# Kernel tuning notes

Measured on AMD Instinct MI355X. Metric: run time of the kernel, lower is better.

The kernel has to match this reference:

```python
import jax, jax.numpy as jnp
import numpy as np

BIAS_VALUE = -1e30


def apply_rope(inputs, positions, max_wavelength=10000):
    # inputs: [B, T, H, Dh]; positions: [B, T]
    head_dim = inputs.shape[-1]
    fraction = 2 * jnp.arange(0, head_dim // 2) / head_dim
    timescale = max_wavelength ** fraction
    sinusoid_inp = positions[..., jnp.newaxis] / timescale[jnp.newaxis, :]  # [B, T, Dh/2]
    sinusoid_inp = sinusoid_inp[..., jnp.newaxis, :]                        # [B, T, 1, Dh/2]
    sin = jnp.sin(sinusoid_inp)
    cos = jnp.cos(sinusoid_inp)
    first_half, second_half = jnp.split(inputs, 2, axis=-1)
    first_part = first_half * cos - second_half * sin
    second_part = second_half * cos + first_half * sin
    return jnp.concatenate([first_part, second_part], axis=-1).astype(inputs.dtype)


def rms_norm(x, scale):
    var = jnp.mean(jnp.square(x), axis=-1, keepdims=True)
    return x * jax.lax.rsqrt(var + 1e-6) * (1 + scale)


def setup_inputs() -> dict:
    key = jax.random.key(0)
    ks = jax.random.split(key, 12)
    B, T, D, H, Dh = 4, 2048, 512, 8, 64
    q = jax.random.normal(ks[0], (B, T, D), jnp.float32)
    kv = jax.random.normal(ks[1], (B, T, D), jnp.float32)
    mask = jnp.broadcast_to(jnp.tril(jnp.ones((T, T), bool))[None, None], (B, 1, T, T))
    pos = jnp.broadcast_to(jnp.arange(T, dtype=jnp.int32), (B, T))
    s = 0.02
    return {
        "q": q, "kv": kv, "mask": mask, "q_positions": pos, "kv_positions": pos,
        "wq": jax.random.normal(ks[2], (D, H * Dh), jnp.float32) * s,
        "bq": jnp.zeros((H * Dh,), jnp.float32),
        "wk": jax.random.normal(ks[3], (D, H * Dh), jnp.float32) * s,
        "bk": jnp.zeros((H * Dh,), jnp.float32),
        "wv": jax.random.normal(ks[4], (D, H * Dh), jnp.float32) * s,
        "bv": jnp.zeros((H * Dh,), jnp.float32),
        "scale_q": jax.random.normal(ks[5], (Dh,), jnp.float32) * s,
        "scale_k": jax.random.normal(ks[6], (Dh,), jnp.float32) * s,
        "wo": jax.random.normal(ks[7], (H * Dh, D), jnp.float32) * s,
        "bo": jnp.zeros((D,), jnp.float32),
    }


def reference(q, kv, mask, q_positions, kv_positions,
              wq, bq, wk, bk, wv, bv, scale_q, scale_k, wo, bo):
    B, T, D = q.shape
    H = 8
    Dh = wq.shape[1] // H
    qk_size = Dh

    def proj(x, w, b):
        y = x @ w + b
        return y.reshape(*x.shape[:-1], H, -1)  # [B, T, H, Dh]

    query_heads = rms_norm(proj(q, wq, bq), scale_q)
    key_heads = rms_norm(proj(kv, wk, bk), scale_k)
    value_heads = proj(kv, wv, bv)

    query_heads = apply_rope(query_heads, q_positions)
    key_heads = apply_rope(key_heads, kv_positions)

    attn_logits = jnp.einsum('bthd,bThd->bhtT', query_heads, key_heads)
    attn_logits = attn_logits / np.sqrt(qk_size).astype(q.dtype)
    attn_logits = jnp.where(mask, attn_logits, BIAS_VALUE)
    attn_weights = jax.nn.softmax(attn_logits, axis=-1)
    attn_weights = jnp.where(mask, attn_weights, 0)
    attn = jnp.einsum('bhtT,bThd->bthd', attn_weights, value_heads)
    attn = attn.reshape(B, T, -1)
    return attn @ wo + bo
```

## Files before the change

### kernel.cpp

```cpp
#include <hip/hip_runtime.h>
#include <hip/hip_bf16.h>
#include <cstdint>

#define B_ 4
#define T_ 2048
#define D_ 512
#define H_ 8

typedef __bf16 bf16x8 __attribute__((ext_vector_type(8)));
typedef __bf16 bf16x4 __attribute__((ext_vector_type(4)));
typedef float f32x4 __attribute__((ext_vector_type(4)));

#define QSCALE 0.18033688011112042f
#define MSHIFT 16.0f

__device__ inline void gload_lds16(const void* g, void* l) {
    __builtin_amdgcn_global_load_lds(
        (const __attribute__((address_space(1))) void*)g,
        (__attribute__((address_space(3))) void*)l, 16, 0, 0);
}

__global__ void cast2_kernel(const float* __restrict__ qf, const float* __restrict__ kvf,
                             __bf16* __restrict__ qb, __bf16* __restrict__ kvb, int n4) {
    int stride = gridDim.x * blockDim.x;
    for (int i = blockIdx.x * blockDim.x + threadIdx.x; i < 2 * n4; i += stride) {
        const float* src = (i < n4) ? qf : kvf;
        __bf16* dst = (i < n4) ? qb : kvb;
        int j = (i < n4) ? i : i - n4;
        float4 v = reinterpret_cast<const float4*>(src)[j];
        bf16x4 o = { (__bf16)v.x, (__bf16)v.y, (__bf16)v.z, (__bf16)v.w };
        reinterpret_cast<bf16x4*>(dst)[j] = o;
    }
}

__global__ void transpose_w4_kernel(const float* __restrict__ wq, const float* __restrict__ wk,
                                    const float* __restrict__ wv, const float* __restrict__ wo,
                                    __bf16* __restrict__ wqkvT, __bf16* __restrict__ woT) {
    __shared__ float tile[32][33];
    int z = blockIdx.z;
    const float* in = (z == 0) ? wq : (z == 1) ? wk : (z == 2) ? wv : wo;
    __bf16* out = (z < 3) ? wqkvT + (size_t)z * D_ * D_ : woT;
    int tx = threadIdx.x & 31, ty = threadIdx.x >> 5;
    int r0 = blockIdx.y * 32, c0 = blockIdx.x * 32;
#pragma unroll
    for (int i = 0; i < 4; i++)
        tile[ty + i * 8][tx] = in[(size_t)(r0 + ty + i * 8) * D_ + c0 + tx];
    __syncthreads();
#pragma unroll
    for (int i = 0; i < 4; i++)
        out[(size_t)(c0 + ty + i * 8) * D_ + r0 + tx] = (__bf16)tile[tx][ty + i * 8];
}

__global__ void rope_table_kernel(float2* __restrict__ tab) {
    int i = blockIdx.x * 256 + threadIdx.x;
    int p = i >> 5, d2 = i & 31;
    float inv_ts = exp2f((float)d2 * (-13.28771237954945f / 32.0f));
    float ang = (float)p * inv_ts;
    float sv, cv;
    __sincosf(ang, &sv, &cv);
    tab[i] = make_float2(cv, sv);
}

template<int MODE>
__global__ __launch_bounds__(256, 2) void gemm_tile_kernel(
    const __bf16* __restrict__ Xq, const __bf16* __restrict__ Xkv,
    const __bf16* __restrict__ WT,
    const float* __restrict__ biasQ, const float* __restrict__ biasK,
    const float* __restrict__ biasV,
    float* __restrict__ outf, __bf16* __restrict__ qh, __bf16* __restrict__ kh,
    __bf16* __restrict__ vt,
    const float* __restrict__ scale_q, const float* __restrict__ scale_k,
    const int* __restrict__ qpos, const int* __restrict__ kpos,
    const float2* __restrict__ rtab, int M, int Ntot, int K) {
    __shared__ __bf16 Ab[2][128 * 32];
    __shared__ __bf16 Bb[2][128 * 32];

    const int tid = threadIdx.x;
    const int lane = tid & 63, widx = tid >> 6;
    const int lo = lane & 15, hi = lane >> 4;
    const int wm = widx >> 1, wn = widx & 1;

    const int nwg = gridDim.x;
    const int q8 = nwg >> 3;
    int bid = blockIdx.x;
    int swz = (bid & 7) * q8 + (bid >> 3);
    const int ntn = Ntot >> 7;
    const int m0 = (swz / ntn) << 7;
    const int nt = swz % ntn;
    const int n0g = nt << 7;
    const int seg = (MODE == 3) ? (nt >> 2) : 0;
    const __bf16* X = (MODE == 3 && seg > 0) ? Xkv : Xq;

    const int srow = tid >> 2;
    const int sslot = tid & 3;

    f32x4 acc[4][4] = {};

    auto stage = [&](int kc, int bufi) {
#pragma unroll
        for (int i = 0; i < 2; i++) {
            int row = i * 64 + srow;
            int cs = sslot ^ ((row >> 1) & 3);
            gload_lds16(X + (size_t)(m0 + row) * K + kc + cs * 8,
                        &Ab[bufi][(i * 64 + widx * 16) * 32]);
        }
#pragma unroll
        for (int i = 0; i < 2; i++) {
            int row = i * 64 + srow;
            int cs = sslot ^ ((row >> 1) & 3);
            gload_lds16(WT + (size_t)(n0g + row) * K + kc + cs * 8,
                        &Bb[bufi][(i * 64 + widx * 16) * 32]);
        }
    };

    const int nks = K >> 5;
    stage(0, 0);
    __syncthreads();
    int cur = 0;

    for (int ks = 0; ks < nks; ks++) {
        if (ks + 1 < nks) stage((ks + 1) << 5, cur ^ 1);

        bf16x8 a[4], bvec[4];
#pragma unroll
        for (int mf = 0; mf < 4; mf++) {
            int R = wm * 64 + mf * 16 + lo;
            a[mf] = *reinterpret_cast<const bf16x8*>(&Ab[cur][R * 32 + ((hi ^ ((R >> 1) & 3)) << 3)]);
        }
#pragma unroll
        for (int nf = 0; nf < 4; nf++) {
            int R = wn * 64 + nf * 16 + lo;
            bvec[nf] = *reinterpret_cast<const bf16x8*>(&Bb[cur][R * 32 + ((hi ^ ((R >> 1) & 3)) << 3)]);
        }
#pragma unroll
        for (int mf = 0; mf < 4; mf++)
#pragma unroll
            for (int nf = 0; nf < 4; nf++)
                acc[mf][nf] = __builtin_amdgcn_mfma_f32_16x16x32_bf16(a[mf], bvec[nf], acc[mf][nf], 0, 0, 0);

        __syncthreads();
        cur ^= 1;
    }

    const int mrow0 = m0 + wm * 64;

    if (MODE == 0) {
        const int ncol0 = n0g + wn * 64;
        float bs[4];
#pragma unroll
        for (int nf = 0; nf < 4; nf++) bs[nf] = biasQ[ncol0 + nf * 16 + lo];
#pragma unroll
        for (int mf = 0; mf < 4; mf++)
#pragma unroll
            for (int nf = 0; nf < 4; nf++)
#pragma unroll
                for (int r = 0; r < 4; r++) {
                    int row = mrow0 + mf * 16 + hi * 4 + r;
                    outf[(size_t)row * Ntot + ncol0 + nf * 16 + lo] = acc[mf][nf][r] + bs[nf];
                }
    } else {
        const int ncol0 = ((nt & 3) << 7) + wn * 64;
        const int h = ncol0 >> 6;
        const float* bias = (seg == 0) ? biasQ : (seg == 1) ? biasK : biasV;
        float bs[4];
#pragma unroll
        for (int nf = 0; nf < 4; nf++) bs[nf] = bias[ncol0 + nf * 16 + lo];

        if (seg < 2) {
            const float* scale = seg ? scale_k : scale_q;
            const int* pos = seg ? kpos : qpos;
            __bf16* dst0 = seg ? kh : qh;
            const float qmul = seg ? 1.0f : QSCALE;
            float sc4[4];
#pragma unroll
            for (int nf = 0; nf < 4; nf++) sc4[nf] = (1.0f + scale[nf * 16 + lo]) * qmul;
#pragma unroll
            for (int mf = 0; mf < 4; mf++) {
#pragma unroll
                for (int r = 0; r < 4; r++) {
                    int row = mrow0 + mf * 16 + hi * 4 + r;
                    float y0 = acc[mf][0][r] + bs[0];
                    float y1 = acc[mf][1][r] + bs[1];
                    float y2 = acc[mf][2][r] + bs[2];
                    float y3 = acc[mf][3][r] + bs[3];
                    float ps = y0 * y0 + y1 * y1 + y2 * y2 + y3 * y3;
#pragma unroll
                    for (int off = 1; off < 16; off <<= 1) ps += __shfl_xor(ps, off);
                    float rmsf = rsqrtf(ps * (1.0f / 64.0f) + 1e-6f);
                    int p = pos[row];
                    float2 c0 = rtab[p * 32 + lo];
                    float2 c1 = rtab[p * 32 + 16 + lo];
                    float z0 = y0 * rmsf * sc4[0];
                    float z1 = y1 * rmsf * sc4[1];
                    float z2 = y2 * rmsf * sc4[2];
                    float z3 = y3 * rmsf * sc4[3];
                    int b = row >> 11, t = row & (T_ - 1);
                    __bf16* dst = dst0 + ((size_t)(b * H_ + h) * T_ + t) * 64;
                    dst[lo]      = (__bf16)(z0 * c0.x - z2 * c0.y);
                    dst[16 + lo] = (__bf16)(z1 * c1.x - z3 * c1.y);
                    dst[32 + lo] = (__bf16)(z2 * c0.x + z0 * c0.y);
                    dst[48 + lo] = (__bf16)(z3 * c1.x + z1 * c1.y);
                }
            }
        } else {
#pragma unroll
            for (int mf = 0; mf < 4; mf++) {
                int row0 = mrow0 + mf * 16 + hi * 4;
                int b = row0 >> 11, t0 = row0 & (T_ - 1);
#pragma unroll
                for (int nf = 0; nf < 4; nf++) {
                    int d = nf * 16 + lo;
                    bf16x4 pk = { (__bf16)(acc[mf][nf][0] + bs[nf]), (__bf16)(acc[mf][nf][1] + bs[nf]),
                                  (__bf16)(acc[mf][nf][2] + bs[nf]), (__bf16)(acc[mf][nf][3] + bs[nf]) };
                    *reinterpret_cast<bf16x4*>(vt + ((size_t)(b * H_ + h) * 64 + d) * T_ + t0) = pk;
                }
            }
        }
    }
}

__global__ __launch_bounds__(256, 3) void attn_kernel(const __bf16* __restrict__ qh,
                                                      const __bf16* __restrict__ kh,
                                                      const __bf16* __restrict__ vt,
                                                      __bf16* __restrict__ attn) {
    __shared__ __bf16 kbuf[2][64 * 64];
    __shared__ __bf16 vbuf[2][64 * 64];
    __shared__ __bf16 plds[4][16][72];

    const int lane = threadIdx.x & 63, widx = threadIdx.x >> 6;
    const int lo = lane & 15, hi = lane >> 4;
    const int bh = blockIdx.x;
    const int sid = 31 - blockIdx.y;
    const int ntiles = sid + 1;
    const int qb = sid * 64 + widx * 16;
    const __bf16* Qg = qh + (size_t)bh * T_ * 64;
    const __bf16* Kg = kh + (size_t)bh * T_ * 64;
    const __bf16* Vg = vt + (size_t)bh * 64 * T_;
    const int b = bh >> 3, h = bh & 7;

    const int srow = lane >> 3;
    const int sslot = lane & 7;
    const int schunk = sslot ^ srow;

    bf16x8 qa[2];
#pragma unroll
    for (int c = 0; c < 2; c++)
        qa[c] = *reinterpret_cast<const bf16x8*>(Qg + (size_t)(qb + lo) * 64 + c * 32 + hi * 8);

    f32x4 o[4] = {};
    float l = 0.0f;
    const f32x4 minit = { -MSHIFT, -MSHIFT, -MSHIFT, -MSHIFT };

    auto stage = [&](int tile, int bufi) {
        const int kvb0 = tile * 64;
#pragma unroll
        for (int i = 0; i < 2; i++) {
            int r = widx * 16 + i * 8 + srow;
            gload_lds16(Kg + (size_t)(kvb0 + r) * 64 + schunk * 8,
                        &kbuf[bufi][(widx * 16 + i * 8) * 64]);
        }
#pragma unroll
        for (int i = 0; i < 2; i++) {
            int r = widx * 16 + i * 8 + srow;
            gload_lds16(Vg + (size_t)r * T_ + kvb0 + schunk * 8,
                        &vbuf[bufi][(widx * 16 + i * 8) * 64]);
        }
    };

    stage(0, 0);
    __syncthreads();
    int cur = 0;

    for (int j = 0; j < ntiles; ++j) {
        if (j + 1 < ntiles) stage(j + 1, cur ^ 1);

        f32x4 s[4] = { minit, minit, minit, minit };
        __builtin_amdgcn_s_setprio(1);
#pragma unroll
        for (int c = 0; c < 2; c++) {
#pragma unroll
            for (int f = 0; f < 4; f++) {
                int R = f * 16 + lo;
                int C = c * 4 + hi;
                bf16x8 kb = *reinterpret_cast<const bf16x8*>(
                    &kbuf[cur][R * 64 + ((C ^ (lo & 7)) << 3)]);
                s[f] = __builtin_amdgcn_mfma_f32_16x16x32_bf16(kb, qa[c], s[f], 0, 0, 0);
            }
        }
        __builtin_amdgcn_s_setprio(0);

        if (j == ntiles - 1) {
#pragma unroll
            for (int f = 0; f < 4; f++)
#pragma unroll
                for (int r = 0; r < 4; r++)
                    if (f * 16 + hi * 4 + r > widx * 16 + lo) s[f][r] = -1e30f;
        }

        float ps = 0.0f;
        bf16x4 pk[4];
#pragma unroll
        for (int f = 0; f < 4; f++) {
#pragma unroll
            for (int r = 0; r < 4; r++) {
                float e = __builtin_amdgcn_exp2f(s[f][r]);
                ps += e;
                pk[f][r] = (__bf16)e;
            }
        }
        ps += __shfl_xor(ps, 16);
        ps += __shfl_xor(ps, 32);
        l += ps;

#pragma unroll
        for (int f = 0; f < 4; f++)
            *reinterpret_cast<bf16x4*>(&plds[widx][lo][f * 16 + hi * 4]) = pk[f];
        bf16x8 pa0 = *reinterpret_cast<const bf16x8*>(&plds[widx][lo][hi * 8]);
        bf16x8 pa1 = *reinterpret_cast<const bf16x8*>(&plds[widx][lo][32 + hi * 8]);

        __builtin_amdgcn_s_setprio(1);
#pragma unroll
        for (int n = 0; n < 4; n++) {
#pragma unroll
            for (int c = 0; c < 2; c++) {
                int R = n * 16 + lo;
                int C = c * 4 + hi;
                bf16x8 vb = *reinterpret_cast<const bf16x8*>(
                    &vbuf[cur][R * 64 + ((C ^ (lo & 7)) << 3)]);
                o[n] = __builtin_amdgcn_mfma_f32_16x16x32_bf16(vb, c ? pa1 : pa0, o[n], 0, 0, 0);
            }
        }
        __builtin_amdgcn_s_setprio(0);

        __syncthreads();
        cur ^= 1;
    }

    const float inv = 1.0f / l;
    const int qrow = qb + lo;
#pragma unroll
    for (int n = 0; n < 4; n++) {
        bf16x4 pko = { (__bf16)(o[n][0] * inv), (__bf16)(o[n][1] * inv),
                       (__bf16)(o[n][2] * inv), (__bf16)(o[n][3] * inv) };
        *reinterpret_cast<bf16x4*>(attn + ((size_t)b * T_ + qrow) * D_ + h * 64 + n * 16 + hi * 4) = pko;
    }
}

extern "C" void kernel_launch(void* const* d_in, const int* in_sizes, int n_in,
                              void* d_out, int out_size, void* d_ws, size_t ws_size,
                              hipStream_t stream) {
    const float* q  = (const float*)d_in[0];
    const float* kv = (const float*)d_in[1];
    const int* qpos = (const int*)d_in[3];
    const int* kpos = (const int*)d_in[4];
    const float* wq = (const float*)d_in[5];
    const float* bq = (const float*)d_in[6];
    const float* wk = (const float*)d_in[7];
    const float* bk = (const float*)d_in[8];
    const float* wv = (const float*)d_in[9];
    const float* bv = (const float*)d_in[10];
    const float* scale_q = (const float*)d_in[11];
    const float* scale_k = (const float*)d_in[12];
    const float* wo = (const float*)d_in[13];
    const float* bo = (const float*)d_in[14];
    float* out = (float*)d_out;

    char* ws = (char*)d_ws;
    size_t off = 0;
    auto alloc = [&](size_t bytes) {
        void* p = ws + off;
        off += (bytes + 255) & ~(size_t)255;
        return p;
    };
    const size_t MD = (size_t)B_ * T_ * D_;
    __bf16* qb16   = (__bf16*)alloc(MD * 2);
    __bf16* kvb16  = (__bf16*)alloc(MD * 2);
    __bf16* wqkvT  = (__bf16*)alloc((size_t)3 * D_ * D_ * 2);
    __bf16* woT    = (__bf16*)alloc((size_t)D_ * D_ * 2);
    __bf16* qh  = (__bf16*)alloc(MD * 2);
    __bf16* kh  = (__bf16*)alloc(MD * 2);
    __bf16* vt  = (__bf16*)alloc(MD * 2);
    float2* rtab = (float2*)alloc((size_t)T_ * 32 * sizeof(float2));
    __bf16* attn = qb16;

    cast2_kernel<<<2048, 256, 0, stream>>>(q, kv, qb16, kvb16, (int)(MD / 4));
    transpose_w4_kernel<<<dim3(16, 16, 4), 256, 0, stream>>>(wq, wk, wv, wo, wqkvT, woT);
    rope_table_kernel<<<(T_ * 32) / 256, 256, 0, stream>>>(rtab);

    const int M = B_ * T_;
    gemm_tile_kernel<3><<<(M / 128) * (3 * D_ / 128), 256, 0, stream>>>(
        qb16, kvb16, wqkvT, bq, bk, bv, nullptr, qh, kh, vt,
        scale_q, scale_k, qpos, kpos, rtab, M, 3 * D_, D_);
    attn_kernel<<<dim3(B_ * H_, 32), 256, 0, stream>>>(qh, kh, vt, attn);
    gemm_tile_kernel<0><<<(M / 128) * (D_ / 128), 256, 0, stream>>>(
        attn, nullptr, woT, bo, nullptr, nullptr, out, nullptr, nullptr, nullptr,
        nullptr, nullptr, nullptr, nullptr, nullptr, M, D_, D_);
}
```

Baseline: 89.36 us.

## Fuse fp32-to-bf16 input cast into QKV GEMM A-tile staging

```diff
diff --git a/kernel.cpp b/kernel.cpp
--- a/kernel.cpp
+++ b/kernel.cpp
@@ -18,19 +18,6 @@
     __builtin_amdgcn_global_load_lds(
         (const __attribute__((address_space(1))) void*)g,
         (__attribute__((address_space(3))) void*)l, 16, 0, 0);
-}
-
-__global__ void cast2_kernel(const float* __restrict__ qf, const float* __restrict__ kvf,
-                             __bf16* __restrict__ qb, __bf16* __restrict__ kvb, int n4) {
-    int stride = gridDim.x * blockDim.x;
-    for (int i = blockIdx.x * blockDim.x + threadIdx.x; i < 2 * n4; i += stride) {
-        const float* src = (i < n4) ? qf : kvf;
-        __bf16* dst = (i < n4) ? qb : kvb;
-        int j = (i < n4) ? i : i - n4;
-        float4 v = reinterpret_cast<const float4*>(src)[j];
-        bf16x4 o = { (__bf16)v.x, (__bf16)v.y, (__bf16)v.z, (__bf16)v.w };
-        reinterpret_cast<bf16x4*>(dst)[j] = o;
-    }
 }
 
 __global__ void transpose_w4_kernel(const float* __restrict__ wq, const float* __restrict__ wk,
@@ -63,7 +50,8 @@
 
 template<int MODE>
 __global__ __launch_bounds__(256, 2) void gemm_tile_kernel(
-    const __bf16* __restrict__ Xq, const __bf16* __restrict__ Xkv,
+    const float* __restrict__ Aq32, const float* __restrict__ Akv32,
+    const __bf16* __restrict__ Xbf,
     const __bf16* __restrict__ WT,
     const float* __restrict__ biasQ, const float* __restrict__ biasK,
     const float* __restrict__ biasV,
@@ -89,21 +77,16 @@
     const int nt = swz % ntn;
     const int n0g = nt << 7;
     const int seg = (MODE == 3) ? (nt >> 2) : 0;
-    const __bf16* X = (MODE == 3 && seg > 0) ? Xkv : Xq;
 
     const int srow = tid >> 2;
     const int sslot = tid & 3;
 
+    const float* Af32 = (MODE == 3) ? ((seg > 0) ? Akv32 : Aq32) : nullptr;
+
     f32x4 acc[4][4] = {};
-
-    auto stage = [&](int kc, int bufi) {
-#pragma unroll
-        for (int i = 0; i < 2; i++) {
-            int row = i * 64 + srow;
-            int cs = sslot ^ ((row >> 1) & 3);
-            gload_lds16(X + (size_t)(m0 + row) * K + kc + cs * 8,
-                        &Ab[bufi][(i * 64 + widx * 16) * 32]);
-        }
+    float4 areg[2][2];
+
+    auto stageB = [&](int kc, int bufi) {
 #pragma unroll
         for (int i = 0; i < 2; i++) {
             int row = i * 64 + srow;
@@ -112,14 +95,51 @@
                         &Bb[bufi][(i * 64 + widx * 16) * 32]);
         }
     };
+    auto stageA_bf = [&](int kc, int bufi) {
+#pragma unroll
+        for (int i = 0; i < 2; i++) {
+            int row = i * 64 + srow;
+            int cs = sslot ^ ((row >> 1) & 3);
+            gload_lds16(Xbf + (size_t)(m0 + row) * K + kc + cs * 8,
+                        &Ab[bufi][(i * 64 + widx * 16) * 32]);
+        }
+    };
+    auto loadA32 = [&](int kc) {
+#pragma unroll
+        for (int i = 0; i < 2; i++) {
+            const float* src = Af32 + (size_t)(m0 + i * 64 + srow) * K + kc + sslot * 8;
+            areg[i][0] = *reinterpret_cast<const float4*>(src);
+            areg[i][1] = *reinterpret_cast<const float4*>(src + 4);
+        }
+    };
+    auto writeA32 = [&](int bufi) {
+#pragma unroll
+        for (int i = 0; i < 2; i++) {
+            int row = i * 64 + srow;
+            bf16x8 v = { (__bf16)areg[i][0].x, (__bf16)areg[i][0].y,
+                         (__bf16)areg[i][0].z, (__bf16)areg[i][0].w,
+                         (__bf16)areg[i][1].x, (__bf16)areg[i][1].y,
+                         (__bf16)areg[i][1].z, (__bf16)areg[i][1].w };
+            *reinterpret_cast<bf16x8*>(
+                &Ab[bufi][row * 32 + ((sslot ^ ((row >> 1) & 3)) << 3)]) = v;
+        }
+    };
 
     const int nks = K >> 5;
-    stage(0, 0);
+    if constexpr (MODE == 3) {
+        loadA32(0); stageB(0, 0); writeA32(0);
+    } else {
+        stageA_bf(0, 0); stageB(0, 0);
+    }
     __syncthreads();
     int cur = 0;
 
     for (int ks = 0; ks < nks; ks++) {
-        if (ks + 1 < nks) stage((ks + 1) << 5, cur ^ 1);
+        const int kc2 = (ks + 1) << 5;
+        if (ks + 1 < nks) {
+            if constexpr (MODE == 3) { loadA32(kc2); stageB(kc2, cur ^ 1); }
+            else { stageA_bf(kc2, cur ^ 1); stageB(kc2, cur ^ 1); }
+        }
 
         bf16x8 a[4], bvec[4];
 #pragma unroll
@@ -138,6 +158,9 @@
             for (int nf = 0; nf < 4; nf++)
                 acc[mf][nf] = __builtin_amdgcn_mfma_f32_16x16x32_bf16(a[mf], bvec[nf], acc[mf][nf], 0, 0, 0);
 
+        if constexpr (MODE == 3) {
+            if (ks + 1 < nks) writeA32(cur ^ 1);
+        }
         __syncthreads();
         cur ^= 1;
     }
@@ -219,13 +242,13 @@
     }
 }
 
-__global__ __launch_bounds__(256, 3) void attn_kernel(const __bf16* __restrict__ qh,
+__global__ __launch_bounds__(256, 4) void attn_kernel(const __bf16* __restrict__ qh,
                                                       const __bf16* __restrict__ kh,
                                                       const __bf16* __restrict__ vt,
                                                       __bf16* __restrict__ attn) {
     __shared__ __bf16 kbuf[2][64 * 64];
     __shared__ __bf16 vbuf[2][64 * 64];
-    __shared__ __bf16 plds[4][16][72];
+    __shared__ __bf16 plds[4][16][64];
 
     const int lane = threadIdx.x & 63, widx = threadIdx.x >> 6;
     const int lo = lane & 15, hi = lane >> 4;
@@ -314,9 +337,10 @@
 
 #pragma unroll
         for (int f = 0; f < 4; f++)
-            *reinterpret_cast<bf16x4*>(&plds[widx][lo][f * 16 + hi * 4]) = pk[f];
-        bf16x8 pa0 = *reinterpret_cast<const bf16x8*>(&plds[widx][lo][hi * 8]);
-        bf16x8 pa1 = *reinterpret_cast<const bf16x8*>(&plds[widx][lo][32 + hi * 8]);
+            *reinterpret_cast<bf16x4*>(
+                &plds[widx][lo][(((f * 2 + (hi >> 1)) ^ (lo & 7)) << 3) + ((hi & 1) << 2)]) = pk[f];
+        bf16x8 pa0 = *reinterpret_cast<const bf16x8*>(&plds[widx][lo][((hi) ^ (lo & 7)) << 3]);
+        bf16x8 pa1 = *reinterpret_cast<const bf16x8*>(&plds[widx][lo][((4 + hi) ^ (lo & 7)) << 3]);
 
         __builtin_amdgcn_s_setprio(1);
 #pragma unroll
@@ -373,26 +397,23 @@
         return p;
     };
     const size_t MD = (size_t)B_ * T_ * D_;
-    __bf16* qb16   = (__bf16*)alloc(MD * 2);
-    __bf16* kvb16  = (__bf16*)alloc(MD * 2);
     __bf16* wqkvT  = (__bf16*)alloc((size_t)3 * D_ * D_ * 2);
     __bf16* woT    = (__bf16*)alloc((size_t)D_ * D_ * 2);
-    __bf16* qh  = (__bf16*)alloc(MD * 2);
-    __bf16* kh  = (__bf16*)alloc(MD * 2);
-    __bf16* vt  = (__bf16*)alloc(MD * 2);
+    __bf16* qh    = (__bf16*)alloc(MD * 2);
+    __bf16* kh    = (__bf16*)alloc(MD * 2);
+    __bf16* vt    = (__bf16*)alloc(MD * 2);
+    __bf16* attnb = (__bf16*)alloc(MD * 2);
     float2* rtab = (float2*)alloc((size_t)T_ * 32 * sizeof(float2));
-    __bf16* attn = qb16;
-
-    cast2_kernel<<<2048, 256, 0, stream>>>(q, kv, qb16, kvb16, (int)(MD / 4));
+
     transpose_w4_kernel<<<dim3(16, 16, 4), 256, 0, stream>>>(wq, wk, wv, wo, wqkvT, woT);
     rope_table_kernel<<<(T_ * 32) / 256, 256, 0, stream>>>(rtab);
 
     const int M = B_ * T_;
     gemm_tile_kernel<3><<<(M / 128) * (3 * D_ / 128), 256, 0, stream>>>(
-        qb16, kvb16, wqkvT, bq, bk, bv, nullptr, qh, kh, vt,
+        q, kv, nullptr, wqkvT, bq, bk, bv, nullptr, qh, kh, vt,
         scale_q, scale_k, qpos, kpos, rtab, M, 3 * D_, D_);
-    attn_kernel<<<dim3(B_ * H_, 32), 256, 0, stream>>>(qh, kh, vt, attn);
+    attn_kernel<<<dim3(B_ * H_, 32), 256, 0, stream>>>(qh, kh, vt, attnb);
     gemm_tile_kernel<0><<<(M / 128) * (D_ / 128), 256, 0, stream>>>(
-        attn, nullptr, woT, bo, nullptr, nullptr, out, nullptr, nullptr, nullptr,
+        nullptr, nullptr, attnb, woT, bo, nullptr, nullptr, out, nullptr, nullptr, nullptr,
         nullptr, nullptr, nullptr, nullptr, nullptr, M, D_, D_);
 }
```

After: 85.58 us. -4.2%, faster.
